# Performance work log

Hardware: AMD Instinct MI355X
Metric: run time of the kernel (lower is better)

## Reference

```python
import jax, jax.numpy as jnp
import numpy as np

B, S, D = 2, 2048, 1024
H, Hd = 16, 64
THD = H * Hd  # total_head_dim
LAMBDA_INIT = 0.8
ROPE_BASE = 10000.0
GN_EPS = 1e-5


def _rope_tables(seq_len, head_dim, dtype):
    inv_freq = 1.0 / (ROPE_BASE ** (jnp.arange(0, head_dim, 2, dtype=jnp.float32) / head_dim))
    t = jnp.arange(seq_len, dtype=jnp.float32)
    freqs = jnp.outer(t, inv_freq)                      # (S, Hd/2)
    emb = jnp.concatenate([freqs, freqs], axis=-1)      # (S, Hd)
    return jnp.cos(emb).astype(dtype), jnp.sin(emb).astype(dtype)


def _rotate_half(x):
    x1, x2 = jnp.split(x, 2, axis=-1)
    return jnp.concatenate([-x2, x1], axis=-1)


def _apply_rope(q, k, cos, sin):
    # q, k: (B, H, S, Hd); cos/sin: (S, Hd)
    cos = cos[None, None, :, :]
    sin = sin[None, None, :, :]
    q = q * cos + _rotate_half(q) * sin
    k = k * cos + _rotate_half(k) * sin
    return q, k


def setup_inputs() -> dict:
    key = jax.random.key(0)
    ks = jax.random.split(key, 8)
    s_in = 1.0 / np.sqrt(D)
    s_out = 1.0 / np.sqrt(THD)
    return {
        "x": jax.random.normal(ks[0], (B, S, D), dtype=jnp.float32),
        "Wq": jax.random.normal(ks[1], (D, 2 * THD), dtype=jnp.float32) * s_in,
        "Wk": jax.random.normal(ks[2], (D, 2 * THD), dtype=jnp.float32) * s_in,
        "Wv": jax.random.normal(ks[3], (D, THD), dtype=jnp.float32) * s_in,
        "Wo": jax.random.normal(ks[4], (THD, D), dtype=jnp.float32) * s_out,
        "lambda_q1": jnp.full((H,), LAMBDA_INIT, dtype=jnp.float32),
        "lambda_k1": jnp.full((H,), LAMBDA_INIT, dtype=jnp.float32),
        "lambda_q2": jnp.full((H,), LAMBDA_INIT, dtype=jnp.float32),
        "lambda_k2": jnp.full((H,), LAMBDA_INIT, dtype=jnp.float32),
        "lambda_init": jnp.asarray(LAMBDA_INIT, dtype=jnp.float32),
        "gn_weight": jnp.ones((THD,), dtype=jnp.float32),
        "gn_bias": jnp.zeros((THD,), dtype=jnp.float32),
    }


def reference(x, Wq, Wk, Wv, Wo, lambda_q1, lambda_k1, lambda_q2, lambda_k2,
              lambda_init, gn_weight, gn_bias):
    b, s, _ = x.shape
    scale = Hd ** -0.5

    q = (x @ Wq).reshape(b, s, 2, H, Hd).transpose(0, 2, 3, 1, 4)  # (B,2,H,S,Hd)
    k = (x @ Wk).reshape(b, s, 2, H, Hd).transpose(0, 2, 3, 1, 4)
    v = (x @ Wv).reshape(b, s, H, Hd).transpose(0, 2, 1, 3)        # (B,H,S,Hd)

    q1, q2 = q[:, 0], q[:, 1]
    k1, k2 = k[:, 0], k[:, 1]

    cos, sin = _rope_tables(s, Hd, x.dtype)
    q1, k1 = _apply_rope(q1, k1, cos, sin)
    q2, k2 = _apply_rope(q2, k2, cos, sin)

    attn1 = jax.nn.softmax(jnp.einsum("bhqd,bhkd->bhqk", q1, k1) * scale, axis=-1)
    attn2 = jax.nn.softmax(jnp.einsum("bhqd,bhkd->bhqk", q2, k2) * scale, axis=-1)

    lam1 = jnp.exp(lambda_q1 * lambda_k1).reshape(1, H, 1, 1)
    lam2 = jnp.exp(lambda_q2 * lambda_k2).reshape(1, H, 1, 1)
    lam_full = lam1 - lam2 + lambda_init

    attn_diff = attn1 - lam_full * attn2
    out = jnp.einsum("bhqk,bhkd->bhqd", attn_diff, v)              # (B,H,S,Hd)
    out = out.transpose(0, 2, 1, 3).reshape(b * s, H, Hd)           # (B*S,H,Hd)

    # GroupNorm with num_groups=H over channels THD: normalize each head's Hd
    mean = out.mean(axis=-1, keepdims=True)
    var = out.var(axis=-1, keepdims=True)
    out = (out - mean) * jax.lax.rsqrt(var + GN_EPS)
    out = out * gn_weight.reshape(H, Hd) + gn_bias.reshape(H, Hd)

    out = out.reshape(b, s, THD) * (1.0 - lambda_init)
    return out @ Wo
```

## Files before the change

kernel.cpp:

```cpp
#include <hip/hip_runtime.h>
#include <hip/hip_fp16.h>
#include <math.h>

#define NH     16
#define HD     64
#define S_LEN  2048
#define THD_   1024
#define SCALE_LOG2E 0.18033688011112042f

typedef __fp16 f16x8 __attribute__((ext_vector_type(8)));
typedef __fp16 f16x4 __attribute__((ext_vector_type(4)));
typedef __fp16 f16x2 __attribute__((ext_vector_type(2)));
typedef float  f32x4 __attribute__((ext_vector_type(4)));


__device__ inline void wt_body(const float* __restrict__ W,
                               __half* __restrict__ WT, int id, int nmask,
                               int nshift) {
  int n = id & nmask;
  int k8 = (id >> nshift) * 8;
  int N = nmask + 1;
  f16x8 h;
#pragma unroll
  for (int j = 0; j < 8; ++j)
    h[j] = (__fp16)W[(size_t)(k8 + j) * N + n];
  *(f16x8*)(WT + (size_t)n * 1024 + k8) = h;
}

__global__ __launch_bounds__(256) void prep_kernel(
    const float* __restrict__ Wq, const float* __restrict__ Wk,
    __half* __restrict__ WqT, __half* __restrict__ WkT,
    float2* __restrict__ tab) {
  int bid = blockIdx.x;
  int t = threadIdx.x;
  if (bid < 1024) {
    wt_body(Wq, WqT, bid * 256 + t, 2047, 11);
  } else if (bid < 2048) {
    wt_body(Wk, WkT, (bid - 1024) * 256 + t, 2047, 11);
  } else {
    int id = (bid - 2048) * 256 + t;
    int p = id & 31;
    int s = id >> 5;
    float inv = expf(-0.28782313662425574f * (float)p);
    float sn, cs;
    sincosf((float)s * inv, &sn, &cs);
    tab[id] = make_float2(cs, sn);
  }
}

template <int MODE>
__global__ __launch_bounds__(256) void mfma_gemm(const void* __restrict__ Ap,
                                                 const void* __restrict__ Bp,
                                                 void* __restrict__ Cp,
                                                 const float2* __restrict__ tab) {
  __shared__ __fp16 As[128][72];
  __shared__ __fp16 Bs[64][72];
  const int t = threadIdx.x;
  const int w = t >> 6, lane = t & 63;
  const int quad = lane >> 4, lqi = lane & 15;
  const int wm = w * 32;
  const int n0 = blockIdx.x * 64, m0 = blockIdx.y * 128;

  f32x4 acc[2][4];
#pragma unroll
  for (int mt = 0; mt < 2; ++mt)
#pragma unroll
    for (int nt = 0; nt < 4; ++nt) acc[mt][nt] = (f32x4){0.f, 0.f, 0.f, 0.f};

  const int srow = t >> 3;
  const int sc8 = (t & 7) * 8;
  const int gn_ = t & 63;
  const int gk0 = (t >> 6) * 8;

  for (int k0 = 0; k0 < 1024; k0 += 64) {
    if (k0) __syncthreads();
    if (MODE == 3) {
      const __half* A16 = (const __half*)Ap;
#pragma unroll
      for (int p = 0; p < 4; ++p) {
        int row = srow + 32 * p;
        *(f16x8*)&As[row][sc8] =
            *(const f16x8*)(A16 + (size_t)(m0 + row) * 1024 + k0 + sc8);
      }
    } else {
      const float* A32 = (const float*)Ap;
#pragma unroll
      for (int p = 0; p < 4; ++p) {
        int row = srow + 32 * p;
        const float* src = A32 + (size_t)(m0 + row) * 1024 + k0 + sc8;
        float4 u = *(const float4*)src;
        float4 v = *(const float4*)(src + 4);
        f16x8 h;
        h[0] = (__fp16)u.x; h[1] = (__fp16)u.y;
        h[2] = (__fp16)u.z; h[3] = (__fp16)u.w;
        h[4] = (__fp16)v.x; h[5] = (__fp16)v.y;
        h[6] = (__fp16)v.z; h[7] = (__fp16)v.w;
        *(f16x8*)&As[row][sc8] = h;
      }
    }
    if (MODE == 2) {
      const float* B32 = (const float*)Bp;
#pragma unroll
      for (int p = 0; p < 2; ++p) {
        int kc = gk0 + 32 * p;
        f16x8 h;
#pragma unroll
        for (int j = 0; j < 8; ++j)
          h[j] = (__fp16)B32[(size_t)(k0 + kc + j) * 1024 + n0 + gn_];
        *(f16x8*)&Bs[gn_][kc] = h;
      }
    } else {
      const __half* B16 = (const __half*)Bp;
      if (srow < 32) {
#pragma unroll
        for (int p = 0; p < 2; ++p) {
          int row = srow + 32 * p;
          *(f16x8*)&Bs[row][sc8] =
              *(const f16x8*)(B16 + (size_t)(n0 + row) * 1024 + k0 + sc8);
        }
      }
    }
    __syncthreads();
#pragma unroll
    for (int ks = 0; ks < 2; ++ks) {
      f16x8 af[2], bf[4];
#pragma unroll
      for (int mt = 0; mt < 2; ++mt)
        af[mt] = *(const f16x8*)&As[wm + mt * 16 + lqi][ks * 32 + quad * 8];
#pragma unroll
      for (int nt = 0; nt < 4; ++nt)
        bf[nt] = *(const f16x8*)&Bs[nt * 16 + lqi][ks * 32 + quad * 8];
#pragma unroll
      for (int mt = 0; mt < 2; ++mt)
#pragma unroll
        for (int nt = 0; nt < 4; ++nt)
          acc[mt][nt] = __builtin_amdgcn_mfma_f32_16x16x32_f16(
              af[mt], bf[nt], acc[mt][nt], 0, 0, 0);
    }
  }

  const int b = m0 >> 11;
  const int s0 = (m0 & 2047) + wm + quad * 4;
  if (MODE == 0 || MODE == 1) {
    __half* dst = (__half*)Cp;
    const int comp = n0 >> 10, hh = (n0 >> 6) & 15;
    __half* base = dst + ((size_t)(b * 2 + comp) * NH + hh) * (size_t)S_LEN * HD;
#pragma unroll
    for (int nt = 0; nt < 2; ++nt) {
      int p = nt * 16 + lqi;
#pragma unroll
      for (int mt = 0; mt < 2; ++mt) {
#pragma unroll
        for (int i = 0; i < 4; ++i) {
          int s = s0 + mt * 16 + i;
          float2 cs = tab[s * 32 + p];
          float x1 = acc[mt][nt][i], x2 = acc[mt][nt + 2][i];
          float y1 = x1 * cs.x - x2 * cs.y;
          float y2 = x2 * cs.x + x1 * cs.y;
          if (MODE == 1) { y1 *= SCALE_LOG2E; y2 *= SCALE_LOG2E; }
          base[(size_t)s * HD + p] = __float2half(y1);
          base[(size_t)s * HD + p + 32] = __float2half(y2);
        }
      }
    }
  } else if (MODE == 2) {
    __half* vt = (__half*)Cp;
    const int hh = n0 >> 6;
#pragma unroll
    for (int nt = 0; nt < 4; ++nt) {
      int hd = nt * 16 + lqi;
      __half* base = vt + (((size_t)b * NH + hh) * HD + hd) * S_LEN;
#pragma unroll
      for (int mt = 0; mt < 2; ++mt) {
        f16x4 hv;
#pragma unroll
        for (int i = 0; i < 4; ++i) hv[i] = (__fp16)acc[mt][nt][i];
        *(f16x4*)(base + s0 + mt * 16) = hv;
      }
    }
  } else {
    float* Co = (float*)Cp;
#pragma unroll
    for (int mt = 0; mt < 2; ++mt)
#pragma unroll
      for (int i = 0; i < 4; ++i) {
        int m = m0 + wm + mt * 16 + quad * 4 + i;
#pragma unroll
        for (int nt = 0; nt < 4; ++nt)
          Co[(size_t)m * 1024 + n0 + nt * 16 + lqi] = acc[mt][nt][i];
      }
  }
}

__global__ __launch_bounds__(256, 2) void attn_kernel(
    const __half* __restrict__ q_h, const __half* __restrict__ k_h,
    const __half* __restrict__ vt_h, float* __restrict__ out,
    const float* __restrict__ lq1, const float* __restrict__ lk1,
    const float* __restrict__ lq2, const float* __restrict__ lk2,
    const float* __restrict__ lam_init_p) {
  __shared__ __half Ks[2][16][512];
  __shared__ __half Vs[2][64][64];

  const int t = threadIdx.x;
  const int w = t >> 6, lane = t & 63;
  const int quad = lane >> 4, lqi = lane & 15;
  const int r7 = lane & 7;
  const int qt = blockIdx.x;
  const int bh = blockIdx.y;
  const int b = bh >> 4, h = bh & 15;

  const size_t c1 = ((size_t)(b * 2 + 0) * NH + h) * (size_t)S_LEN * HD;
  const size_t c2 = ((size_t)(b * 2 + 1) * NH + h) * (size_t)S_LEN * HD;
  const size_t vtb = ((size_t)b * NH + h) * (size_t)HD * S_LEN;
  const int q0 = qt * 128 + w * 32;

  f16x8 qf[2][2][2];
#pragma unroll
  for (int nt = 0; nt < 2; ++nt)
#pragma unroll
    for (int ks = 0; ks < 2; ++ks) {
      size_t a = (size_t)(q0 + nt * 16 + lqi) * HD + ks * 32 + quad * 8;
      qf[0][nt][ks] = *(const f16x8*)(q_h + c1 + a);
      qf[1][nt][ks] = *(const f16x8*)(q_h + c2 + a);
    }

  f32x4 O[2][4][2];
#pragma unroll
  for (int s = 0; s < 2; ++s)
#pragma unroll
    for (int hm = 0; hm < 4; ++hm)
#pragma unroll
      for (int nt = 0; nt < 2; ++nt) O[s][hm][nt] = (f32x4){0.f, 0.f, 0.f, 0.f};
  float lsum[2][2] = {{0.f, 0.f}, {0.f, 0.f}};

  auto k_src = [&](int c, int k0) -> const __half* {
    if (c < 16) {
      int str = c >> 3, mt = (c >> 1) & 3, ks = c & 1;
      return k_h + (str ? c2 : c1) + (size_t)(k0 + mt * 16 + lqi) * HD +
             ks * 32 + quad * 8;
    }
    int cc = c - 16;
    return vt_h + vtb + (size_t)(cc * 8 + (lane >> 3)) * S_LEN + k0 +
           (lane & 7) * 8;
  };
  auto lds_dst = [&](int c, int buf) -> __half* {
    if (c < 16) return &Ks[buf][c][lane * 8];
    int cc = c - 16;
    int row = cc * 8 + (lane >> 3);
    int col = ((lane & 7) ^ (lane >> 3)) * 8;
    return &Vs[buf][row][col];
  };

  f16x8 r[6];
#pragma unroll
  for (int ci = 0; ci < 6; ++ci) r[ci] = *(const f16x8*)k_src(w + ci * 4, 0);
#pragma unroll
  for (int ci = 0; ci < 6; ++ci) *(f16x8*)lds_dst(w + ci * 4, 0) = r[ci];
  __syncthreads();

  for (int kt = 0; kt < 32; ++kt) {
    const int cur = kt & 1;
    if (kt < 31) {
#pragma unroll
      for (int ci = 0; ci < 6; ++ci)
        r[ci] = *(const f16x8*)k_src(w + ci * 4, (kt + 1) * 64);
    }

#pragma unroll
    for (int g = 0; g < 2; ++g) {
      f16x8 vf[4];
#pragma unroll
      for (int hm = 0; hm < 4; ++hm) {
        const __half* vrow = &Vs[cur][hm * 16 + lqi][0];
        int s0 = (g * 4 + (quad >> 1)) ^ r7;
        int s1 = (g * 4 + 2 + (quad >> 1)) ^ r7;
        union { f16x8 v8; f16x4 v4[2]; } u;
        u.v4[0] = *(const f16x4*)(vrow + s0 * 8 + (quad & 1) * 4);
        u.v4[1] = *(const f16x4*)(vrow + s1 * 8 + (quad & 1) * 4);
        vf[hm] = u.v8;
      }
      f16x8 bfrag[2][2];
#pragma unroll
      for (int str = 0; str < 2; ++str) {
        f16x8 kf00 = *(const f16x8*)&Ks[cur][str * 8 + g * 4 + 0][lane * 8];
        f16x8 kf01 = *(const f16x8*)&Ks[cur][str * 8 + g * 4 + 1][lane * 8];
        f16x8 kf10 = *(const f16x8*)&Ks[cur][str * 8 + g * 4 + 2][lane * 8];
        f16x8 kf11 = *(const f16x8*)&Ks[cur][str * 8 + g * 4 + 3][lane * 8];
#pragma unroll
        for (int nt = 0; nt < 2; ++nt) {
          f32x4 sa = (f32x4){0.f, 0.f, 0.f, 0.f};
          f32x4 sb = (f32x4){0.f, 0.f, 0.f, 0.f};
          sa = __builtin_amdgcn_mfma_f32_16x16x32_f16(kf00, qf[str][nt][0], sa,
                                                      0, 0, 0);
          sa = __builtin_amdgcn_mfma_f32_16x16x32_f16(kf01, qf[str][nt][1], sa,
                                                      0, 0, 0);
          sb = __builtin_amdgcn_mfma_f32_16x16x32_f16(kf10, qf[str][nt][0], sb,
                                                      0, 0, 0);
          sb = __builtin_amdgcn_mfma_f32_16x16x32_f16(kf11, qf[str][nt][1], sb,
                                                      0, 0, 0);
          float ea0 = __builtin_amdgcn_exp2f(sa[0]);
          float ea1 = __builtin_amdgcn_exp2f(sa[1]);
          float ea2 = __builtin_amdgcn_exp2f(sa[2]);
          float ea3 = __builtin_amdgcn_exp2f(sa[3]);
          float eb0 = __builtin_amdgcn_exp2f(sb[0]);
          float eb1 = __builtin_amdgcn_exp2f(sb[1]);
          float eb2 = __builtin_amdgcn_exp2f(sb[2]);
          float eb3 = __builtin_amdgcn_exp2f(sb[3]);
          lsum[str][nt] += ((ea0 + ea1) + (ea2 + ea3)) +
                           ((eb0 + eb1) + (eb2 + eb3));
          union { f16x8 v; f16x2 h2[4]; } pu;
          pu.h2[0] = __builtin_amdgcn_cvt_pkrtz(ea0, ea1);
          pu.h2[1] = __builtin_amdgcn_cvt_pkrtz(ea2, ea3);
          pu.h2[2] = __builtin_amdgcn_cvt_pkrtz(eb0, eb1);
          pu.h2[3] = __builtin_amdgcn_cvt_pkrtz(eb2, eb3);
          bfrag[str][nt] = pu.v;
        }
      }
#pragma unroll
      for (int hm = 0; hm < 4; ++hm)
#pragma unroll
        for (int str = 0; str < 2; ++str)
#pragma unroll
          for (int nt = 0; nt < 2; ++nt)
            O[str][hm][nt] = __builtin_amdgcn_mfma_f32_16x16x32_f16(
                vf[hm], bfrag[str][nt], O[str][hm][nt], 0, 0, 0);
    }

    if (kt < 31) {
#pragma unroll
      for (int ci = 0; ci < 6; ++ci)
        *(f16x8*)lds_dst(w + ci * 4, cur ^ 1) = r[ci];
      __syncthreads();
    }
  }

  const float lam0 = lam_init_p[0];
  const float lam = expf(lq1[h] * lk1[h]) - expf(lq2[h] * lk2[h]) + lam0;
#pragma unroll
  for (int str = 0; str < 2; ++str)
#pragma unroll
    for (int nt = 0; nt < 2; ++nt) {
      float v = lsum[str][nt];
      v += __shfl_xor(v, 16);
      v += __shfl_xor(v, 32);
      lsum[str][nt] = v;
    }
#pragma unroll
  for (int nt = 0; nt < 2; ++nt) {
    float il1 = 1.f / lsum[0][nt];
    float il2 = lam / lsum[1][nt];
    int q = q0 + nt * 16 + lqi;
#pragma unroll
    for (int hm = 0; hm < 4; ++hm) {
      f32x4 o;
#pragma unroll
      for (int i = 0; i < 4; ++i)
        o[i] = O[0][hm][nt][i] * il1 - O[1][hm][nt][i] * il2;
      *(f32x4*)(out + ((size_t)(b * S_LEN + q)) * THD_ + h * HD + hm * 16 +
                quad * 4) = o;
    }
  }
}

__global__ __launch_bounds__(256) void gn_wt_kernel(
    const float* __restrict__ src, __half* __restrict__ dst,
    const float* __restrict__ gw, const float* __restrict__ gb,
    const float* __restrict__ lam_init_p, const float* __restrict__ Wo,
    __half* __restrict__ WoT) {
  if (blockIdx.x >= 16384) {
    wt_body(Wo, WoT, (blockIdx.x - 16384) * 256 + threadIdx.x, 1023, 10);
    return;
  }
  int g = blockIdx.x * 4 + (threadIdx.x >> 6);
  int lane = threadIdx.x & 63;
  float v = src[(size_t)g * 64 + lane];
  float s = v, sq = v * v;
#pragma unroll
  for (int off = 32; off; off >>= 1) {
    s += __shfl_xor(s, off);
    sq += __shfl_xor(sq, off);
  }
  float mean = s * (1.f / 64.f);
  float var = sq * (1.f / 64.f) - mean * mean;
  float rs = rsqrtf(var + 1e-5f);
  int h = g & 15;
  float w = gw[h * 64 + lane], bb = gb[h * 64 + lane];
  dst[(size_t)g * 64 + lane] =
      __float2half(((v - mean) * rs * w + bb) * (1.f - lam_init_p[0]));
}

extern "C" void kernel_launch(void* const* d_in, const int* in_sizes, int n_in,
                              void* d_out, int out_size, void* d_ws,
                              size_t ws_size, hipStream_t stream) {
  const float* x = (const float*)d_in[0];
  const float* Wq = (const float*)d_in[1];
  const float* Wk = (const float*)d_in[2];
  const float* Wv = (const float*)d_in[3];
  const float* Wo = (const float*)d_in[4];
  const float* lq1 = (const float*)d_in[5];
  const float* lk1 = (const float*)d_in[6];
  const float* lq2 = (const float*)d_in[7];
  const float* lk2 = (const float*)d_in[8];
  const float* lam_init = (const float*)d_in[9];
  const float* gnw = (const float*)d_in[10];
  const float* gnb = (const float*)d_in[11];
  float* out = (float*)d_out;

  __half* q_h = (__half*)d_ws;
  __half* k_h = q_h + 8388608;
  __half* vt_h = k_h + 8388608;
  __half* WqT = k_h;
  __half* WkT = vt_h;
  float2* tab = (float2*)(vt_h + 2097152);
  __half* WoT = q_h;
  __half* gn_h = q_h + 1048576;

  dim3 blk(256);
  prep_kernel<<<2304, blk, 0, stream>>>(Wq, Wk, WqT, WkT, tab);
  mfma_gemm<1><<<dim3(32, 32), blk, 0, stream>>>(x, WqT, q_h, tab);
  mfma_gemm<0><<<dim3(32, 32), blk, 0, stream>>>(x, WkT, k_h, tab);
  mfma_gemm<2><<<dim3(16, 32), blk, 0, stream>>>(x, Wv, vt_h, nullptr);
  attn_kernel<<<dim3(16, 32), blk, 0, stream>>>(q_h, k_h, vt_h, out, lq1, lk1,
                                                lq2, lk2, lam_init);
  gn_wt_kernel<<<16896, blk, 0, stream>>>(out, gn_h, gnw, gnb, lam_init, Wo,
                                          WoT);
  mfma_gemm<3><<<dim3(16, 32), blk, 0, stream>>>(gn_h, WoT, out, nullptr);
}
```

Baseline: 337.2 us.

## Halve attention query tile per block and single-buffer V to raise occupancy

Each warp now handles 16 query rows instead of 32, so a block covers 64 queries and the grid doubles to 32x32 blocks. Launch bounds rise to 4 blocks per CU, and the V tile in shared memory becomes single-buffered: each iteration loads V into registers before a barrier, then an extra sync guards the overwrite. The aim is more resident waves and parallelism for latency hiding. In exchange, K/V tiles are re-read from global memory twice as often, each loaded tile feeds fewer MFMAs, and every iteration carries an extra barrier.

Result: slower. 461.0 us (+36.7%).

```diff
diff --git a/kernel.cpp b/kernel.cpp
--- a/kernel.cpp
+++ b/kernel.cpp
@@ -192,14 +192,14 @@
   }
 }
 
-__global__ __launch_bounds__(256, 2) void attn_kernel(
+__global__ __launch_bounds__(256, 4) void attn_kernel(
     const __half* __restrict__ q_h, const __half* __restrict__ k_h,
     const __half* __restrict__ vt_h, float* __restrict__ out,
     const float* __restrict__ lq1, const float* __restrict__ lk1,
     const float* __restrict__ lq2, const float* __restrict__ lk2,
     const float* __restrict__ lam_init_p) {
   __shared__ __half Ks[2][16][512];
-  __shared__ __half Vs[2][64][64];
+  __shared__ __half Vs[64][64];
 
   const int t = threadIdx.x;
   const int w = t >> 6, lane = t & 63;
@@ -212,26 +212,22 @@
   const size_t c1 = ((size_t)(b * 2 + 0) * NH + h) * (size_t)S_LEN * HD;
   const size_t c2 = ((size_t)(b * 2 + 1) * NH + h) * (size_t)S_LEN * HD;
   const size_t vtb = ((size_t)b * NH + h) * (size_t)HD * S_LEN;
-  const int q0 = qt * 128 + w * 32;
-
-  f16x8 qf[2][2][2];
-#pragma unroll
-  for (int nt = 0; nt < 2; ++nt)
-#pragma unroll
-    for (int ks = 0; ks < 2; ++ks) {
-      size_t a = (size_t)(q0 + nt * 16 + lqi) * HD + ks * 32 + quad * 8;
-      qf[0][nt][ks] = *(const f16x8*)(q_h + c1 + a);
-      qf[1][nt][ks] = *(const f16x8*)(q_h + c2 + a);
-    }
-
-  f32x4 O[2][4][2];
+  const int q0 = qt * 64 + w * 16;
+
+  f16x8 qf[2][2];
+#pragma unroll
+  for (int ks = 0; ks < 2; ++ks) {
+    size_t a = (size_t)(q0 + lqi) * HD + ks * 32 + quad * 8;
+    qf[0][ks] = *(const f16x8*)(q_h + c1 + a);
+    qf[1][ks] = *(const f16x8*)(q_h + c2 + a);
+  }
+
+  f32x4 O[2][4];
 #pragma unroll
   for (int s = 0; s < 2; ++s)
 #pragma unroll
-    for (int hm = 0; hm < 4; ++hm)
-#pragma unroll
-      for (int nt = 0; nt < 2; ++nt) O[s][hm][nt] = (f32x4){0.f, 0.f, 0.f, 0.f};
-  float lsum[2][2] = {{0.f, 0.f}, {0.f, 0.f}};
+    for (int hm = 0; hm < 4; ++hm) O[s][hm] = (f32x4){0.f, 0.f, 0.f, 0.f};
+  float lsum[2] = {0.f, 0.f};
 
   auto k_src = [&](int c, int k0) -> const __half* {
     if (c < 16) {
@@ -248,7 +244,7 @@
     int cc = c - 16;
     int row = cc * 8 + (lane >> 3);
     int col = ((lane & 7) ^ (lane >> 3)) * 8;
-    return &Vs[buf][row][col];
+    return &Vs[row][col];
   };
 
   f16x8 r[6];
@@ -260,105 +256,95 @@
 
   for (int kt = 0; kt < 32; ++kt) {
     const int cur = kt & 1;
-    if (kt < 31) {
-#pragma unroll
-      for (int ci = 0; ci < 6; ++ci)
-        r[ci] = *(const f16x8*)k_src(w + ci * 4, (kt + 1) * 64);
-    }
-
-#pragma unroll
-    for (int g = 0; g < 2; ++g) {
-      f16x8 vf[4];
+    f16x8 vf[2][4];
+#pragma unroll
+    for (int g = 0; g < 2; ++g)
 #pragma unroll
       for (int hm = 0; hm < 4; ++hm) {
-        const __half* vrow = &Vs[cur][hm * 16 + lqi][0];
+        const __half* vrow = &Vs[hm * 16 + lqi][0];
         int s0 = (g * 4 + (quad >> 1)) ^ r7;
         int s1 = (g * 4 + 2 + (quad >> 1)) ^ r7;
         union { f16x8 v8; f16x4 v4[2]; } u;
         u.v4[0] = *(const f16x4*)(vrow + s0 * 8 + (quad & 1) * 4);
         u.v4[1] = *(const f16x4*)(vrow + s1 * 8 + (quad & 1) * 4);
-        vf[hm] = u.v8;
-      }
-      f16x8 bfrag[2][2];
+        vf[g][hm] = u.v8;
+      }
+    __syncthreads();
+
+    if (kt < 31) {
+#pragma unroll
+      for (int ci = 0; ci < 6; ++ci)
+        r[ci] = *(const f16x8*)k_src(w + ci * 4, (kt + 1) * 64);
+    }
+
+#pragma unroll
+    for (int g = 0; g < 2; ++g) {
 #pragma unroll
       for (int str = 0; str < 2; ++str) {
         f16x8 kf00 = *(const f16x8*)&Ks[cur][str * 8 + g * 4 + 0][lane * 8];
         f16x8 kf01 = *(const f16x8*)&Ks[cur][str * 8 + g * 4 + 1][lane * 8];
         f16x8 kf10 = *(const f16x8*)&Ks[cur][str * 8 + g * 4 + 2][lane * 8];
         f16x8 kf11 = *(const f16x8*)&Ks[cur][str * 8 + g * 4 + 3][lane * 8];
-#pragma unroll
-        for (int nt = 0; nt < 2; ++nt) {
-          f32x4 sa = (f32x4){0.f, 0.f, 0.f, 0.f};
-          f32x4 sb = (f32x4){0.f, 0.f, 0.f, 0.f};
-          sa = __builtin_amdgcn_mfma_f32_16x16x32_f16(kf00, qf[str][nt][0], sa,
-                                                      0, 0, 0);
-          sa = __builtin_amdgcn_mfma_f32_16x16x32_f16(kf01, qf[str][nt][1], sa,
-                                                      0, 0, 0);
-          sb = __builtin_amdgcn_mfma_f32_16x16x32_f16(kf10, qf[str][nt][0], sb,
-                                                      0, 0, 0);
-          sb = __builtin_amdgcn_mfma_f32_16x16x32_f16(kf11, qf[str][nt][1], sb,
-                                                      0, 0, 0);
-          float ea0 = __builtin_amdgcn_exp2f(sa[0]);
-          float ea1 = __builtin_amdgcn_exp2f(sa[1]);
-          float ea2 = __builtin_amdgcn_exp2f(sa[2]);
-          float ea3 = __builtin_amdgcn_exp2f(sa[3]);
-          float eb0 = __builtin_amdgcn_exp2f(sb[0]);
-          float eb1 = __builtin_amdgcn_exp2f(sb[1]);
-          float eb2 = __builtin_amdgcn_exp2f(sb[2]);
-          float eb3 = __builtin_amdgcn_exp2f(sb[3]);
-          lsum[str][nt] += ((ea0 + ea1) + (ea2 + ea3)) +
-                           ((eb0 + eb1) + (eb2 + eb3));
-          union { f16x8 v; f16x2 h2[4]; } pu;
-          pu.h2[0] = __builtin_amdgcn_cvt_pkrtz(ea0, ea1);
-          pu.h2[1] = __builtin_amdgcn_cvt_pkrtz(ea2, ea3);
-          pu.h2[2] = __builtin_amdgcn_cvt_pkrtz(eb0, eb1);
-          pu.h2[3] = __builtin_amdgcn_cvt_pkrtz(eb2, eb3);
-          bfrag[str][nt] = pu.v;
-        }
-      }
-#pragma unroll
-      for (int hm = 0; hm < 4; ++hm)
-#pragma unroll
-        for (int str = 0; str < 2; ++str)
-#pragma unroll
-          for (int nt = 0; nt < 2; ++nt)
-            O[str][hm][nt] = __builtin_amdgcn_mfma_f32_16x16x32_f16(
-                vf[hm], bfrag[str][nt], O[str][hm][nt], 0, 0, 0);
+        f32x4 sa = (f32x4){0.f, 0.f, 0.f, 0.f};
+        f32x4 sb = (f32x4){0.f, 0.f, 0.f, 0.f};
+        sa = __builtin_amdgcn_mfma_f32_16x16x32_f16(kf00, qf[str][0], sa,
+                                                    0, 0, 0);
+        sa = __builtin_amdgcn_mfma_f32_16x16x32_f16(kf01, qf[str][1], sa,
+                                                    0, 0, 0);
+        sb = __builtin_amdgcn_mfma_f32_16x16x32_f16(kf10, qf[str][0], sb,
+                                                    0, 0, 0);
+        sb = __builtin_amdgcn_mfma_f32_16x16x32_f16(kf11, qf[str][1], sb,
+                                                    0, 0, 0);
+        float ea0 = __builtin_amdgcn_exp2f(sa[0]);
+        float ea1 = __builtin_amdgcn_exp2f(sa[1]);
+        float ea2 = __builtin_amdgcn_exp2f(sa[2]);
+        float ea3 = __builtin_amdgcn_exp2f(sa[3]);
+        float eb0 = __builtin_amdgcn_exp2f(sb[0]);
+        float eb1 = __builtin_amdgcn_exp2f(sb[1]);
+        float eb2 = __builtin_amdgcn_exp2f(sb[2]);
+        float eb3 = __builtin_amdgcn_exp2f(sb[3]);
+        lsum[str] += ((ea0 + ea1) + (ea2 + ea3)) +
+                     ((eb0 + eb1) + (eb2 + eb3));
+        union { f16x8 v; f16x2 h2[4]; } pu;
+        pu.h2[0] = __builtin_amdgcn_cvt_pkrtz(ea0, ea1);
+        pu.h2[1] = __builtin_amdgcn_cvt_pkrtz(ea2, ea3);
+        pu.h2[2] = __builtin_amdgcn_cvt_pkrtz(eb0, eb1);
+        pu.h2[3] = __builtin_amdgcn_cvt_pkrtz(eb2, eb3);
+#pragma unroll
+        for (int hm = 0; hm < 4; ++hm)
+          O[str][hm] = __builtin_amdgcn_mfma_f32_16x16x32_f16(
+              vf[g][hm], pu.v, O[str][hm], 0, 0, 0);
+      }
     }
 
     if (kt < 31) {
 #pragma unroll
       for (int ci = 0; ci < 6; ++ci)
         *(f16x8*)lds_dst(w + ci * 4, cur ^ 1) = r[ci];
-      __syncthreads();
-    }
+    }
+    __syncthreads();
   }
 
   const float lam0 = lam_init_p[0];
   const float lam = expf(lq1[h] * lk1[h]) - expf(lq2[h] * lk2[h]) + lam0;
 #pragma unroll
-  for (int str = 0; str < 2; ++str)
-#pragma unroll
-    for (int nt = 0; nt < 2; ++nt) {
-      float v = lsum[str][nt];
-      v += __shfl_xor(v, 16);
-      v += __shfl_xor(v, 32);
-      lsum[str][nt] = v;
-    }
-#pragma unroll
-  for (int nt = 0; nt < 2; ++nt) {
-    float il1 = 1.f / lsum[0][nt];
-    float il2 = lam / lsum[1][nt];
-    int q = q0 + nt * 16 + lqi;
-#pragma unroll
-    for (int hm = 0; hm < 4; ++hm) {
-      f32x4 o;
-#pragma unroll
-      for (int i = 0; i < 4; ++i)
-        o[i] = O[0][hm][nt][i] * il1 - O[1][hm][nt][i] * il2;
-      *(f32x4*)(out + ((size_t)(b * S_LEN + q)) * THD_ + h * HD + hm * 16 +
-                quad * 4) = o;
-    }
+  for (int str = 0; str < 2; ++str) {
+    float v = lsum[str];
+    v += __shfl_xor(v, 16);
+    v += __shfl_xor(v, 32);
+    lsum[str] = v;
+  }
+  float il1 = 1.f / lsum[0];
+  float il2 = lam / lsum[1];
+  int q = q0 + lqi;
+#pragma unroll
+  for (int hm = 0; hm < 4; ++hm) {
+    f32x4 o;
+#pragma unroll
+    for (int i = 0; i < 4; ++i)
+      o[i] = O[0][hm][i] * il1 - O[1][hm][i] * il2;
+    *(f32x4*)(out + ((size_t)(b * S_LEN + q)) * THD_ + h * HD + hm * 16 +
+              quad * 4) = o;
   }
 }
 
@@ -420,7 +406,7 @@
   mfma_gemm<1><<<dim3(32, 32), blk, 0, stream>>>(x, WqT, q_h, tab);
   mfma_gemm<0><<<dim3(32, 32), blk, 0, stream>>>(x, WkT, k_h, tab);
   mfma_gemm<2><<<dim3(16, 32), blk, 0, stream>>>(x, Wv, vt_h, nullptr);
-  attn_kernel<<<dim3(16, 32), blk, 0, stream>>>(q_h, k_h, vt_h, out, lq1, lk1,
+  attn_kernel<<<dim3(32, 32), blk, 0, stream>>>(q_h, k_h, vt_h, out, lq1, lk1,
                                                 lq2, lk2, lam_init);
   gn_wt_kernel<<<16896, blk, 0, stream>>>(out, gn_h, gnw, gnb, lam_init, Wo,
                                           WoT);
```
